# Optimization experiments

Hardware: AMD Instinct MI355X
Metric: run time of the kernel (lower is better)

Reference implementation:

```python
import jax, jax.numpy as jnp
import numpy as np

K, Q, DIM = 64, 128, 1024
TF_W, DE_W, FFT_W = 1.0, 0.8, 0.6  # opt.TF_weight / DE_weight / FFT_weight


def setup_inputs() -> dict:
    key = jax.random.key(0)
    ks = jax.random.split(key, 9)
    def feats(k):
        return jax.random.normal(k, (K, Q, DIM), dtype=jnp.float32)
    def protos(k):
        return jax.random.normal(k, (K, DIM), dtype=jnp.float32)
    def var(k):
        # positive variances, bounded away from zero
        return jax.random.uniform(k, (K,), dtype=jnp.float32) + 0.5
    return {
        "TFq_output": feats(ks[0]), "TFs_proto": protos(ks[1]), "TF_variance": var(ks[2]),
        "DEq_output": feats(ks[3]), "DEs_proto": protos(ks[4]), "DE_variance": var(ks[5]),
        "FFTq_output": feats(ks[6]), "FFTs_proto": protos(ks[7]), "FFT_variance": var(ks[8]),
    }


def _mah_dist(xq, proto, variance):
    # ||x - p||^2 / var via expansion: avoids materializing (num, protonum, dim)
    x2 = jnp.sum(xq * xq, axis=1, keepdims=True)            # (num, 1)
    p2 = jnp.sum(proto * proto, axis=1)[None, :]            # (1, protonum)
    xp = xq @ proto.T                                       # (num, protonum)
    return (x2 - 2.0 * xp + p2) / variance[None, :]


def _modality(xq, proto, variance, w):
    logits = -_mah_dist(xq, proto, variance)
    pred = w * jax.nn.softmax(logits, axis=1)
    mahloss = -(w * jax.nn.log_softmax(logits, axis=1))
    return pred, mahloss


def reference(TFq_output, TFs_proto, TF_variance,
              DEq_output, DEs_proto, DE_variance,
              FFTq_output, FFTs_proto, FFT_variance):
    k, q, _ = TFq_output.shape
    y = jnp.repeat(jnp.arange(k), q)                         # (k*q,)

    tf_pred, tf_loss = _modality(TFq_output.reshape(k * q, -1), TFs_proto, TF_variance, TF_W)
    de_pred, de_loss = _modality(DEq_output.reshape(k * q, -1), DEs_proto, DE_variance, DE_W)
    fft_pred, fft_loss = _modality(FFTq_output.reshape(k * q, -1), FFTs_proto, FFT_variance, FFT_W)

    fusion_loss = tf_loss + de_loss + fft_loss               # (k*q, k)
    loss = jnp.take_along_axis(fusion_loss, y[:, None], axis=1).squeeze(-1).mean()

    pred_mah = tf_pred + de_pred + fft_pred
    pred = jnp.argmax(pred_mah, axis=1)
    acc = (pred == y).astype(jnp.float32).mean()
    return (loss, acc)
```

## Files before the change

kernel.cpp:

```cpp
#include <hip/hip_runtime.h>


typedef _Float16 half8 __attribute__((ext_vector_type(8)));
typedef float    floatx4 __attribute__((ext_vector_type(4)));

#define NCLS   64
#define QPC    128
#define DIM    1024
#define NROWS  (NCLS * QPC)
#define NRT    (NROWS / 16)
#define UW2    132

#define OFF_W     0
#define W_BYTES   (3 * NCLS * DIM * 2)
#define OFF_P2    W_BYTES
#define OFF_PD    397312
#define PD_BYTES  (3 * NRT * 2 * 16 * 64 * 4)
#define OFF_PX2   (OFF_PD + PD_BYTES)
#define PX2_BYTES (3 * NRT * 2 * 16 * 4)
#define OFF_LP    (OFF_PX2 + PX2_BYTES)
#define OFF_CP    (OFF_LP + NRT * 4)
#define WS_NEED   (OFF_CP + NRT * 4)

__device__ __forceinline__ void dma4(const float* g, float* l) {
    __builtin_amdgcn_global_load_lds(
        (const __attribute__((address_space(1))) void*)g,
        (__attribute__((address_space(3))) void*)l,
        4, 0, 0);
}

__global__ __launch_bounds__(64) void prep_protos(
    const float* __restrict__ Ptf, const float* __restrict__ Pde,
    const float* __restrict__ Pff, _Float16* __restrict__ W,
    float* __restrict__ p2)
{
    const int m    = blockIdx.x >> 5;
    const int kcg  = blockIdx.x & 31;
    const int lane = threadIdx.x;
    const int l15  = lane & 15;
    const int quad = lane >> 4;
    const float* __restrict__ P = (m == 0) ? Ptf : (m == 1) ? Pde : Pff;

    #pragma unroll
    for (int t = 0; t < 4; ++t) {
        const float* src = P + (size_t)(t * 16 + l15) * DIM + kcg * 32 + quad * 8;
        const float4 b0 = *reinterpret_cast<const float4*>(src);
        const float4 b1 = *reinterpret_cast<const float4*>(src + 4);
        half8 h;
        h[0] = (_Float16)b0.x; h[1] = (_Float16)b0.y;
        h[2] = (_Float16)b0.z; h[3] = (_Float16)b0.w;
        h[4] = (_Float16)b1.x; h[5] = (_Float16)b1.y;
        h[6] = (_Float16)b1.z; h[7] = (_Float16)b1.w;
        *reinterpret_cast<half8*>(W + ((size_t)(m * 32 + kcg) * 4 + t) * 512 + lane * 8) = h;

        float s = b0.x*b0.x + b0.y*b0.y + b0.z*b0.z + b0.w*b0.w
                + b1.x*b1.x + b1.y*b1.y + b1.z*b1.z + b1.w*b1.w;
        s += __shfl_xor(s, 16);
        s += __shfl_xor(s, 32);
        if (quad == 0) atomicAdd(&p2[m * 64 + t * 16 + l15], s);
    }
}

__global__ __launch_bounds__(256, 8) void fusion_main(
    const float* __restrict__ Xtf, const float* __restrict__ Xde,
    const float* __restrict__ Xff, const _Float16* __restrict__ W,
    float* __restrict__ pd, float* __restrict__ px2)
{
    __shared__ float buf[2][16 * UW2];

    const int tid  = threadIdx.x;
    const int w    = tid >> 6;
    const int lane = tid & 63;
    const int l15  = lane & 15;
    const int quad = lane >> 4;
    const int b    = blockIdx.x;
    const int m    = b >> 10;
    const int rt   = (b & 1023) >> 1;
    const int ks   = b & 1;
    const int rowBase = rt * 16;

    const float* __restrict__ X = (m == 0) ? Xtf : (m == 1) ? Xde : Xff;

    const float* gb = X + (size_t)(rowBase + w * 4) * DIM + ks * 512 + lane;

    floatx4 d = (floatx4){0.f, 0.f, 0.f, 0.f};
    float x2p = 0.0f;

    #pragma unroll
    for (int r4 = 0; r4 < 4; ++r4) {
        dma4(gb + (size_t)r4 * DIM,      &buf[0][(w * 4 + r4) * UW2]);
        dma4(gb + (size_t)r4 * DIM + 64, &buf[0][(w * 4 + r4) * UW2 + 64]);
    }

    #pragma unroll
    for (int c = 0; c < 4; ++c) {
        __syncthreads();
        if (c < 3) {
            const float* g1 = gb + (c + 1) * 128;
            float* lb = &buf[(c + 1) & 1][0];
            #pragma unroll
            for (int r4 = 0; r4 < 4; ++r4) {
                dma4(g1 + (size_t)r4 * DIM,      lb + (w * 4 + r4) * UW2);
                dma4(g1 + (size_t)r4 * DIM + 64, lb + (w * 4 + r4) * UW2 + 64);
            }
        }
        const float* tb = &buf[c & 1][0];
        #pragma unroll
        for (int kc = 0; kc < 4; ++kc) {
            const int off = l15 * UW2 + kc * 32 + quad * 8;
            const float4 a0 = *reinterpret_cast<const float4*>(tb + off);
            const float4 a1 = *reinterpret_cast<const float4*>(tb + off + 4);
            const int kcg = ks * 16 + c * 4 + kc;
            const half8 bf = *reinterpret_cast<const half8*>(
                W + ((size_t)(m * 32 + kcg) * 4 + w) * 512 + lane * 8);

            if (w == 0)
                x2p += a0.x*a0.x + a0.y*a0.y + a0.z*a0.z + a0.w*a0.w
                     + a1.x*a1.x + a1.y*a1.y + a1.z*a1.z + a1.w*a1.w;

            half8 af;
            af[0] = (_Float16)a0.x; af[1] = (_Float16)a0.y;
            af[2] = (_Float16)a0.z; af[3] = (_Float16)a0.w;
            af[4] = (_Float16)a1.x; af[5] = (_Float16)a1.y;
            af[6] = (_Float16)a1.z; af[7] = (_Float16)a1.w;

            d = __builtin_amdgcn_mfma_f32_16x16x32_f16(af, bf, d, 0, 0, 0);
        }
    }

    const size_t tb2 = (size_t)((m * NRT + rt) * 2 + ks);
    if (w == 0) {
        x2p += __shfl_xor(x2p, 16);
        x2p += __shfl_xor(x2p, 32);
        if (quad == 0) px2[tb2 * 16 + l15] = x2p;
    }

    float* o = pd + tb2 * 1024;
    #pragma unroll
    for (int r = 0; r < 4; ++r)
        o[(quad * 4 + r) * 64 + w * 16 + l15] = d[r];
}

__global__ __launch_bounds__(256) void finalize1(
    const float* __restrict__ pd, const float* __restrict__ px2,
    const float* __restrict__ p2g,
    const float* __restrict__ Vtf, const float* __restrict__ Vde,
    const float* __restrict__ Vff,
    float* __restrict__ lossPart, float* __restrict__ cntPart)
{
    const int rt   = blockIdx.x;
    const int tid  = threadIdx.x;
    const int v    = tid >> 6;
    const int lane = tid & 63;

    float loss = 0.0f, cnt = 0.0f;
    #pragma unroll
    for (int r4 = 0; r4 < 4; ++r4) {
        const int row = v * 4 + r4;
        const int R   = rt * 16 + row;
        const int y   = R >> 7;
        float pf = 0.0f;
        #pragma unroll
        for (int m = 0; m < 3; ++m) {
            const size_t t0 = (size_t)((m * NRT + rt) * 2);
            const float dsum = pd[t0 * 1024 + row * 64 + lane]
                             + pd[(t0 + 1) * 1024 + row * 64 + lane];
            const float x2 = px2[t0 * 16 + row] + px2[(t0 + 1) * 16 + row];
            const float* __restrict__ V = (m == 0) ? Vtf : (m == 1) ? Vde : Vff;
            const float wgt = (m == 0) ? 1.0f : (m == 1) ? 0.8f : 0.6f;

            const float lg = (2.0f * dsum - x2 - p2g[m * 64 + lane]) / V[lane];
            float mx = lg;
            #pragma unroll
            for (int dl = 1; dl <= 32; dl <<= 1) mx = fmaxf(mx, __shfl_xor(mx, dl));
            float s = expf(lg - mx);
            #pragma unroll
            for (int dl = 1; dl <= 32; dl <<= 1) s += __shfl_xor(s, dl);
            const float lse = mx + logf(s);

            if (lane == y) loss += wgt * (lse - lg);
            pf += wgt * expf(lg - lse);
        }
        float bv = pf; int bc = lane;
        #pragma unroll
        for (int dl = 1; dl <= 32; dl <<= 1) {
            const float ov = __shfl_xor(bv, dl);
            const int   oc = __shfl_xor(bc, dl);
            if (ov > bv || (ov == bv && oc < bc)) { bv = ov; bc = oc; }
        }
        if (lane == 0 && bc == y) cnt += 1.0f;
    }

    #pragma unroll
    for (int dl = 1; dl <= 32; dl <<= 1) {
        loss += __shfl_xor(loss, dl);
        cnt  += __shfl_xor(cnt, dl);
    }
    __shared__ float sl[4], sc[4];
    if (lane == 0) { sl[v] = loss; sc[v] = cnt; }
    __syncthreads();
    if (tid == 0) {
        lossPart[rt] = sl[0] + sl[1] + sl[2] + sl[3];
        cntPart[rt]  = sc[0] + sc[1] + sc[2] + sc[3];
    }
}

__global__ __launch_bounds__(256) void finalize2(
    const float* __restrict__ lossPart, const float* __restrict__ cntPart,
    float* __restrict__ out)
{
    const int tid  = threadIdx.x;
    const int lane = tid & 63;
    const int v    = tid >> 6;
    float l = 0.0f, c = 0.0f;
    for (int i = tid; i < NRT; i += 256) { l += lossPart[i]; c += cntPart[i]; }
    #pragma unroll
    for (int dl = 1; dl <= 32; dl <<= 1) {
        l += __shfl_xor(l, dl);
        c += __shfl_xor(c, dl);
    }
    __shared__ float sl[4], sc[4];
    if (lane == 0) { sl[v] = l; sc[v] = c; }
    __syncthreads();
    if (tid == 0) {
        out[0] = (sl[0] + sl[1] + sl[2] + sl[3]) * (1.0f / NROWS);
        out[1] = (sc[0] + sc[1] + sc[2] + sc[3]) * (1.0f / NROWS);
    }
}

#define NWAVES 12
#define KSPLIT 4
#define KSLICE (DIM / KSPLIT)
#define NITER  (KSLICE / 32)
#define DSTRIDE 17
#define PSTRIDE 65

__global__ __launch_bounds__(NWAVES * 64) void fusion_loss_fallback(
    const float* __restrict__ Xtf, const float* __restrict__ Ptf, const float* __restrict__ Vtf,
    const float* __restrict__ Xde, const float* __restrict__ Pde, const float* __restrict__ Vde,
    const float* __restrict__ Xff, const float* __restrict__ Pff, const float* __restrict__ Vff,
    float* __restrict__ out)
{
    __shared__ float dpart[NWAVES][64 * DSTRIDE];
    __shared__ float x2part[NWAVES][16];
    __shared__ float p2part[NWAVES][64];
    __shared__ float predL[16 * PSTRIDE];
    __shared__ float lossL;

    const int tid  = threadIdx.x;
    const int wave = tid >> 6;
    const int lane = tid & 63;
    const int l15  = lane & 15;
    const int quad = lane >> 4;
    const int m    = wave >> 2;
    const int kq   = wave & 3;
    const int rowBase = blockIdx.x * 16;

    for (int i = tid; i < 16 * PSTRIDE; i += NWAVES * 64) predL[i] = 0.0f;
    if (tid == 0) lossL = 0.0f;

    const float* __restrict__ X = (m == 0) ? Xtf : (m == 1) ? Xde : Xff;
    const float* __restrict__ P = (m == 0) ? Ptf : (m == 1) ? Pde : Pff;
    const float* __restrict__ V = (m == 0) ? Vtf : (m == 1) ? Vde : Vff;
    const float  w = (m == 0) ? 1.0f : (m == 1) ? 0.8f : 0.6f;

    floatx4 d[4];
    #pragma unroll
    for (int t = 0; t < 4; ++t) d[t] = (floatx4){0.f, 0.f, 0.f, 0.f};
    float x2p    = 0.0f;
    float p2p[4] = {0.f, 0.f, 0.f, 0.f};

    const float* xrow = X + (size_t)(rowBase + l15) * DIM + kq * KSLICE + quad * 8;
    const float* prow[4];
    #pragma unroll
    for (int t = 0; t < 4; ++t)
        prow[t] = P + (size_t)(t * 16 + l15) * DIM + kq * KSLICE + quad * 8;

    #pragma unroll 2
    for (int kc = 0; kc < NITER; ++kc) {
        const int ko = kc * 32;
        const float4 a0 = *reinterpret_cast<const float4*>(xrow + ko);
        const float4 a1 = *reinterpret_cast<const float4*>(xrow + ko + 4);
        float4 b0[4], b1[4];
        #pragma unroll
        for (int t = 0; t < 4; ++t) {
            b0[t] = *reinterpret_cast<const float4*>(prow[t] + ko);
            b1[t] = *reinterpret_cast<const float4*>(prow[t] + ko + 4);
        }
        x2p += a0.x*a0.x + a0.y*a0.y + a0.z*a0.z + a0.w*a0.w
             + a1.x*a1.x + a1.y*a1.y + a1.z*a1.z + a1.w*a1.w;
        half8 af;
        af[0] = (_Float16)a0.x; af[1] = (_Float16)a0.y;
        af[2] = (_Float16)a0.z; af[3] = (_Float16)a0.w;
        af[4] = (_Float16)a1.x; af[5] = (_Float16)a1.y;
        af[6] = (_Float16)a1.z; af[7] = (_Float16)a1.w;
        #pragma unroll
        for (int t = 0; t < 4; ++t) {
            p2p[t] += b0[t].x*b0[t].x + b0[t].y*b0[t].y + b0[t].z*b0[t].z + b0[t].w*b0[t].w
                    + b1[t].x*b1[t].x + b1[t].y*b1[t].y + b1[t].z*b1[t].z + b1[t].w*b1[t].w;
            half8 bf;
            bf[0] = (_Float16)b0[t].x; bf[1] = (_Float16)b0[t].y;
            bf[2] = (_Float16)b0[t].z; bf[3] = (_Float16)b0[t].w;
            bf[4] = (_Float16)b1[t].x; bf[5] = (_Float16)b1[t].y;
            bf[6] = (_Float16)b1[t].z; bf[7] = (_Float16)b1[t].w;
            d[t] = __builtin_amdgcn_mfma_f32_16x16x32_f16(af, bf, d[t], 0, 0, 0);
        }
    }

    x2p += __shfl_xor(x2p, 16);
    x2p += __shfl_xor(x2p, 32);
    #pragma unroll
    for (int t = 0; t < 4; ++t) {
        p2p[t] += __shfl_xor(p2p[t], 16);
        p2p[t] += __shfl_xor(p2p[t], 32);
    }
    {
        float* dp = &dpart[wave][lane * DSTRIDE];
        #pragma unroll
        for (int t = 0; t < 4; ++t)
            *reinterpret_cast<float4*>(dp + t * 4) =
                make_float4(d[t][0], d[t][1], d[t][2], d[t][3]);
        if (quad == 0) {
            x2part[wave][l15] = x2p;
            #pragma unroll
            for (int t = 0; t < 4; ++t) p2part[wave][t * 16 + l15] = p2p[t];
        }
    }
    __syncthreads();

    const int y = rowBase >> 7;

    if (kq == 0) {
        floatx4 dsum[4];
        #pragma unroll
        for (int t = 0; t < 4; ++t) dsum[t] = (floatx4){0.f, 0.f, 0.f, 0.f};
        float x2r[4] = {0.f, 0.f, 0.f, 0.f};
        float p2c[4] = {0.f, 0.f, 0.f, 0.f};
        #pragma unroll
        for (int k2 = 0; k2 < KSPLIT; ++k2) {
            const int wv = m * 4 + k2;
            const float* src = &dpart[wv][lane * DSTRIDE];
            #pragma unroll
            for (int t = 0; t < 4; ++t) {
                const float4 vv = *reinterpret_cast<const float4*>(src + t * 4);
                dsum[t][0] += vv.x; dsum[t][1] += vv.y; dsum[t][2] += vv.z; dsum[t][3] += vv.w;
            }
            #pragma unroll
            for (int r = 0; r < 4; ++r) x2r[r] += x2part[wv][quad * 4 + r];
            #pragma unroll
            for (int t = 0; t < 4; ++t) p2c[t] += p2part[wv][t * 16 + l15];
        }
        float vc[4];
        #pragma unroll
        for (int t = 0; t < 4; ++t) vc[t] = V[t * 16 + l15];

        float lossAcc = 0.0f;
        #pragma unroll
        for (int r = 0; r < 4; ++r) {
            float lg[4];
            #pragma unroll
            for (int t = 0; t < 4; ++t)
                lg[t] = (2.0f * dsum[t][r] - x2r[r] - p2c[t]) / vc[t];
            float mx = fmaxf(fmaxf(lg[0], lg[1]), fmaxf(lg[2], lg[3]));
            #pragma unroll
            for (int dl = 1; dl <= 8; dl <<= 1) mx = fmaxf(mx, __shfl_xor(mx, dl));
            float s = expf(lg[0] - mx) + expf(lg[1] - mx)
                    + expf(lg[2] - mx) + expf(lg[3] - mx);
            #pragma unroll
            for (int dl = 1; dl <= 8; dl <<= 1) s += __shfl_xor(s, dl);
            const float lse = mx + logf(s);
            const int row = quad * 4 + r;
            #pragma unroll
            for (int t = 0; t < 4; ++t) {
                const int colc = t * 16 + l15;
                if (colc == y) lossAcc += w * (lse - lg[t]);
                atomicAdd(&predL[row * PSTRIDE + colc], w * expf(lg[t] - lse));
            }
        }
        #pragma unroll
        for (int dl = 1; dl <= 32; dl <<= 1) lossAcc += __shfl_xor(lossAcc, dl);
        if (lane == 0) atomicAdd(&lossL, lossAcc);
    }
    __syncthreads();

    if (wave == 0) {
        float cnt = 0.0f;
        #pragma unroll 1
        for (int r = 0; r < 16; ++r) {
            float bv = predL[r * PSTRIDE + lane];
            int   bc = lane;
            #pragma unroll
            for (int dl = 1; dl <= 32; dl <<= 1) {
                const float ov = __shfl_xor(bv, dl);
                const int   oc = __shfl_xor(bc, dl);
                if (ov > bv || (ov == bv && oc < bc)) { bv = ov; bc = oc; }
            }
            if (lane == 0 && bc == y) cnt += 1.0f;
        }
        if (lane == 0) {
            atomicAdd(&out[0], lossL * (1.0f / NROWS));
            atomicAdd(&out[1], cnt * (1.0f / NROWS));
        }
    }
}

extern "C" void kernel_launch(void* const* d_in, const int* in_sizes, int n_in,
                              void* d_out, int out_size, void* d_ws, size_t ws_size,
                              hipStream_t stream) {
    const float* Xtf = (const float*)d_in[0];
    const float* Ptf = (const float*)d_in[1];
    const float* Vtf = (const float*)d_in[2];
    const float* Xde = (const float*)d_in[3];
    const float* Pde = (const float*)d_in[4];
    const float* Vde = (const float*)d_in[5];
    const float* Xff = (const float*)d_in[6];
    const float* Pff = (const float*)d_in[7];
    const float* Vff = (const float*)d_in[8];
    float* out = (float*)d_out;

    if (ws_size >= (size_t)WS_NEED) {
        char* ws = (char*)d_ws;
        _Float16* W     = (_Float16*)(ws + OFF_W);
        float*    p2    = (float*)(ws + OFF_P2);
        float*    pd    = (float*)(ws + OFF_PD);
        float*    px2   = (float*)(ws + OFF_PX2);
        float*    lossP = (float*)(ws + OFF_LP);
        float*    cntP  = (float*)(ws + OFF_CP);

        hipMemsetAsync(p2, 0, 3 * NCLS * sizeof(float), stream);
        prep_protos<<<dim3(96), dim3(64), 0, stream>>>(Ptf, Pde, Pff, W, p2);
        fusion_main<<<dim3(3 * NRT * 2), dim3(256), 0, stream>>>(
            Xtf, Xde, Xff, W, pd, px2);
        finalize1<<<dim3(NRT), dim3(256), 0, stream>>>(
            pd, px2, p2, Vtf, Vde, Vff, lossP, cntP);
        finalize2<<<dim3(1), dim3(256), 0, stream>>>(lossP, cntP, out);
    } else {
        hipMemsetAsync(out, 0, 2 * sizeof(float), stream);
        fusion_loss_fallback<<<dim3(NROWS / 16), dim3(NWAVES * 64), 0, stream>>>(
            Xtf, Ptf, Vtf, Xde, Pde, Vde, Xff, Pff, Vff, out);
    }
}
```

Baseline: 156.8 us.

## Fuse per-modality softmax/loss into GEMM kernel, drop K-split partials

The main kernel no longer splits the K dimension across two blocks. Each block now covers the full 1024-wide reduction for a 16-row tile and computes logits, the softmax, the log-sum-exp and the per-modality loss in its epilogue, writing weighted probabilities and per-block loss partials. The finalize pass shrinks to summing the three modality predictions and taking the argmax. This removes the partial dot-product and x2 buffers and the duplicated softmax work in finalize, but it halves the number of main-kernel blocks and lengthens each block's serial loop, which can reduce parallelism and latency hiding.

```diff
diff --git a/kernel.cpp b/kernel.cpp
--- a/kernel.cpp
+++ b/kernel.cpp
@@ -11,16 +11,14 @@
 #define NRT    (NROWS / 16)
 #define UW2    132
 
-#define OFF_W     0
-#define W_BYTES   (3 * NCLS * DIM * 2)
-#define OFF_P2    W_BYTES
-#define OFF_PD    397312
-#define PD_BYTES  (3 * NRT * 2 * 16 * 64 * 4)
-#define OFF_PX2   (OFF_PD + PD_BYTES)
-#define PX2_BYTES (3 * NRT * 2 * 16 * 4)
-#define OFF_LP    (OFF_PX2 + PX2_BYTES)
-#define OFF_CP    (OFF_LP + NRT * 4)
-#define WS_NEED   (OFF_CP + NRT * 4)
+#define OFF_W      0
+#define W_BYTES    (3 * NCLS * DIM * 2)
+#define OFF_P2     W_BYTES
+#define OFF_PRED   397312
+#define PRED_BYTES (3 * NROWS * NCLS * 4)
+#define OFF_LP     (OFF_PRED + PRED_BYTES)
+#define OFF_CP     (OFF_LP + 3 * NRT * 4)
+#define WS_NEED    (OFF_CP + NRT * 4)
 
 __device__ __forceinline__ void dma4(const float* g, float* l) {
     __builtin_amdgcn_global_load_lds(
@@ -63,10 +61,18 @@
 
 __global__ __launch_bounds__(256, 8) void fusion_main(
     const float* __restrict__ Xtf, const float* __restrict__ Xde,
-    const float* __restrict__ Xff, const _Float16* __restrict__ W,
-    float* __restrict__ pd, float* __restrict__ px2)
+    const float* __restrict__ Xff,
+    const float* __restrict__ Vtf, const float* __restrict__ Vde,
+    const float* __restrict__ Vff,
+    const _Float16* __restrict__ W, const float* __restrict__ p2g,
+    float* __restrict__ predOut,
+    float* __restrict__ lossPart)
 {
     __shared__ float buf[2][16 * UW2];
+    __shared__ float x2s[16];
+    __shared__ float mxW[4][16];
+    __shared__ float sW[4][16];
+    __shared__ float lossW[4];
 
     const int tid  = threadIdx.x;
     const int w    = tid >> 6;
@@ -74,14 +80,15 @@
     const int l15  = lane & 15;
     const int quad = lane >> 4;
     const int b    = blockIdx.x;
-    const int m    = b >> 10;
-    const int rt   = (b & 1023) >> 1;
-    const int ks   = b & 1;
+    const int m    = b >> 9;
+    const int rt   = b & 511;
     const int rowBase = rt * 16;
 
     const float* __restrict__ X = (m == 0) ? Xtf : (m == 1) ? Xde : Xff;
-
-    const float* gb = X + (size_t)(rowBase + w * 4) * DIM + ks * 512 + lane;
+    const float* __restrict__ V = (m == 0) ? Vtf : (m == 1) ? Vde : Vff;
+    const float  wgt = (m == 0) ? 1.0f : (m == 1) ? 0.8f : 0.6f;
+
+    const float* gb = X + (size_t)(rowBase + w * 4) * DIM + lane;
 
     floatx4 d = (floatx4){0.f, 0.f, 0.f, 0.f};
     float x2p = 0.0f;
@@ -93,9 +100,9 @@
     }
 
     #pragma unroll
-    for (int c = 0; c < 4; ++c) {
+    for (int c = 0; c < 8; ++c) {
         __syncthreads();
-        if (c < 3) {
+        if (c < 7) {
             const float* g1 = gb + (c + 1) * 128;
             float* lb = &buf[(c + 1) & 1][0];
             #pragma unroll
@@ -110,7 +117,7 @@
             const int off = l15 * UW2 + kc * 32 + quad * 8;
             const float4 a0 = *reinterpret_cast<const float4*>(tb + off);
             const float4 a1 = *reinterpret_cast<const float4*>(tb + off + 4);
-            const int kcg = ks * 16 + c * 4 + kc;
+            const int kcg = c * 4 + kc;
             const half8 bf = *reinterpret_cast<const half8*>(
                 W + ((size_t)(m * 32 + kcg) * 4 + w) * 512 + lane * 8);
 
@@ -128,60 +135,78 @@
         }
     }
 
-    const size_t tb2 = (size_t)((m * NRT + rt) * 2 + ks);
     if (w == 0) {
         x2p += __shfl_xor(x2p, 16);
         x2p += __shfl_xor(x2p, 32);
-        if (quad == 0) px2[tb2 * 16 + l15] = x2p;
-    }
-
-    float* o = pd + tb2 * 1024;
+        if (quad == 0) x2s[l15] = x2p;
+    }
+    __syncthreads();
+
+    const int col = w * 16 + l15;
+    const float vc  = V[col];
+    const float p2c = p2g[m * 64 + col];
+    float lg[4];
     #pragma unroll
     for (int r = 0; r < 4; ++r)
-        o[(quad * 4 + r) * 64 + w * 16 + l15] = d[r];
+        lg[r] = (2.0f * d[r] - x2s[quad * 4 + r] - p2c) / vc;
+
+    #pragma unroll
+    for (int r = 0; r < 4; ++r) {
+        float mx = lg[r];
+        #pragma unroll
+        for (int dl = 1; dl <= 8; dl <<= 1) mx = fmaxf(mx, __shfl_xor(mx, dl));
+        if (l15 == 0) mxW[w][quad * 4 + r] = mx;
+    }
+    __syncthreads();
+
+    float gmx[4];
+    #pragma unroll
+    for (int r = 0; r < 4; ++r) {
+        const int row = quad * 4 + r;
+        gmx[r] = fmaxf(fmaxf(mxW[0][row], mxW[1][row]),
+                       fmaxf(mxW[2][row], mxW[3][row]));
+        float s = expf(lg[r] - gmx[r]);
+        #pragma unroll
+        for (int dl = 1; dl <= 8; dl <<= 1) s += __shfl_xor(s, dl);
+        if (l15 == 0) sW[w][quad * 4 + r] = s;
+    }
+    __syncthreads();
+
+    const int y = rowBase >> 7;
+    float lossAcc = 0.0f;
+    #pragma unroll
+    for (int r = 0; r < 4; ++r) {
+        const int row = quad * 4 + r;
+        const float lse = gmx[r] + logf(sW[0][row] + sW[1][row]
+                                      + sW[2][row] + sW[3][row]);
+        if (col == y) lossAcc += wgt * (lse - lg[r]);
+        predOut[((size_t)m * NROWS + rowBase + row) * 64 + col] =
+            wgt * expf(lg[r] - lse);
+    }
+    #pragma unroll
+    for (int dl = 1; dl <= 32; dl <<= 1) lossAcc += __shfl_xor(lossAcc, dl);
+    if (lane == 0) lossW[w] = lossAcc;
+    __syncthreads();
+    if (tid == 0) lossPart[b] = lossW[0] + lossW[1] + lossW[2] + lossW[3];
 }
 
 __global__ __launch_bounds__(256) void finalize1(
-    const float* __restrict__ pd, const float* __restrict__ px2,
-    const float* __restrict__ p2g,
-    const float* __restrict__ Vtf, const float* __restrict__ Vde,
-    const float* __restrict__ Vff,
-    float* __restrict__ lossPart, float* __restrict__ cntPart)
+    const float* __restrict__ pred, float* __restrict__ cntPart)
 {
     const int rt   = blockIdx.x;
     const int tid  = threadIdx.x;
     const int v    = tid >> 6;
     const int lane = tid & 63;
 
-    float loss = 0.0f, cnt = 0.0f;
+    float cnt = 0.0f;
     #pragma unroll
     for (int r4 = 0; r4 < 4; ++r4) {
-        const int row = v * 4 + r4;
-        const int R   = rt * 16 + row;
-        const int y   = R >> 7;
-        float pf = 0.0f;
-        #pragma unroll
-        for (int m = 0; m < 3; ++m) {
-            const size_t t0 = (size_t)((m * NRT + rt) * 2);
-            const float dsum = pd[t0 * 1024 + row * 64 + lane]
-                             + pd[(t0 + 1) * 1024 + row * 64 + lane];
-            const float x2 = px2[t0 * 16 + row] + px2[(t0 + 1) * 16 + row];
-            const float* __restrict__ V = (m == 0) ? Vtf : (m == 1) ? Vde : Vff;
-            const float wgt = (m == 0) ? 1.0f : (m == 1) ? 0.8f : 0.6f;
-
-            const float lg = (2.0f * dsum - x2 - p2g[m * 64 + lane]) / V[lane];
-            float mx = lg;
-            #pragma unroll
-            for (int dl = 1; dl <= 32; dl <<= 1) mx = fmaxf(mx, __shfl_xor(mx, dl));
-            float s = expf(lg - mx);
-            #pragma unroll
-            for (int dl = 1; dl <= 32; dl <<= 1) s += __shfl_xor(s, dl);
-            const float lse = mx + logf(s);
-
-            if (lane == y) loss += wgt * (lse - lg);
-            pf += wgt * expf(lg - lse);
-        }
-        float bv = pf; int bc = lane;
+        const int R = rt * 16 + v * 4 + r4;
+        const int y = R >> 7;
+        float p = pred[(size_t)R * 64 + lane]
+                + pred[((size_t)NROWS + R) * 64 + lane]
+                + pred[((size_t)2 * NROWS + R) * 64 + lane];
+        float bv = p; int bc = lane;
         #pragma unroll
         for (int dl = 1; dl <= 32; dl <<= 1) {
             const float ov = __shfl_xor(bv, dl);
@@ -190,19 +215,12 @@
         }
         if (lane == 0 && bc == y) cnt += 1.0f;
     }
-
-    #pragma unroll
-    for (int dl = 1; dl <= 32; dl <<= 1) {
-        loss += __shfl_xor(loss, dl);
-        cnt  += __shfl_xor(cnt, dl);
-    }
-    __shared__ float sl[4], sc[4];
-    if (lane == 0) { sl[v] = loss; sc[v] = cnt; }
-    __syncthreads();
-    if (tid == 0) {
-        lossPart[rt] = sl[0] + sl[1] + sl[2] + sl[3];
-        cntPart[rt]  = sc[0] + sc[1] + sc[2] + sc[3];
-    }
+    #pragma unroll
+    for (int dl = 1; dl <= 32; dl <<= 1) cnt += __shfl_xor(cnt, dl);
+    __shared__ float sc[4];
+    if (lane == 0) sc[v] = cnt;
+    __syncthreads();
+    if (tid == 0) cntPart[rt] = sc[0] + sc[1] + sc[2] + sc[3];
 }
 
 __global__ __launch_bounds__(256) void finalize2(
@@ -213,7 +231,8 @@
     const int lane = tid & 63;
     const int v    = tid >> 6;
     float l = 0.0f, c = 0.0f;
-    for (int i = tid; i < NRT; i += 256) { l += lossPart[i]; c += cntPart[i]; }
+    for (int i = tid; i < 3 * NRT; i += 256) l += lossPart[i];
+    for (int i = tid; i < NRT; i += 256)     c += cntPart[i];
     #pragma unroll
     for (int dl = 1; dl <= 32; dl <<= 1) {
         l += __shfl_xor(l, dl);
@@ -422,17 +441,15 @@
         char* ws = (char*)d_ws;
         _Float16* W     = (_Float16*)(ws + OFF_W);
         float*    p2    = (float*)(ws + OFF_P2);
-        float*    pd    = (float*)(ws + OFF_PD);
-        float*    px2   = (float*)(ws + OFF_PX2);
+        float*    pred  = (float*)(ws + OFF_PRED);
         float*    lossP = (float*)(ws + OFF_LP);
         float*    cntP  = (float*)(ws + OFF_CP);
 
         hipMemsetAsync(p2, 0, 3 * NCLS * sizeof(float), stream);
         prep_protos<<<dim3(96), dim3(64), 0, stream>>>(Ptf, Pde, Pff, W, p2);
-        fusion_main<<<dim3(3 * NRT * 2), dim3(256), 0, stream>>>(
-            Xtf, Xde, Xff, W, pd, px2);
-        finalize1<<<dim3(NRT), dim3(256), 0, stream>>>(
-            pd, px2, p2, Vtf, Vde, Vff, lossP, cntP);
+        fusion_main<<<dim3(3 * NRT), dim3(256), 0, stream>>>(
+            Xtf, Xde, Xff, Vtf, Vde, Vff, W, p2, pred, lossP);
+        finalize1<<<dim3(NRT), dim3(256), 0, stream>>>(pred, cntP);
         finalize2<<<dim3(1), dim3(256), 0, stream>>>(lossP, cntP, out);
     } else {
         hipMemsetAsync(out, 0, 2 * sizeof(float), stream);
```

Result: faster. 153.6 us (-2.0%).
